# Kernel optimization log

Hardware: AMD Instinct MI355X
Metric: run time of the kernel (lower is better)

Reference implementation:

```python
import jax, jax.numpy as jnp
import numpy as np

IGNORE_LABEL_ID = -100
GRID = 40                 # grid_width
PATH = 6                  # path_token_id
SP_W = 10.0               # spatial_penalty_weight
CONN_W = 5.0              # connectivity_weight
SEQ = GRID * GRID         # 1600
BIG = SEQ                 # sentinel larger than any flat index


def _spatial_penalty(pred):
    """Vectorized version of spatial_connectivity_loss's per-batch python loop.
    For each predicted path token, find the NEXT path token in flat order and
    penalize Manhattan jumps > 1. pred: [B, SEQ] int."""
    B = pred.shape[0]
    mask = pred == PATH                                   # [B,S]
    idx = jnp.arange(SEQ, dtype=jnp.int32)
    cand = jnp.where(mask, idx[None, :], BIG)
    # nxt[b,i] = smallest path index >= i (reverse cumulative min)
    nxt = jax.lax.cummin(cand, axis=1, reverse=True)
    # next path index strictly after i
    nxt_after = jnp.concatenate([nxt[:, 1:], jnp.full((B, 1), BIG, nxt.dtype)], axis=1)
    valid = mask & (nxt_after < BIG)                      # pairs (i, next)
    p2 = jnp.minimum(nxt_after, SEQ - 1)                  # keep indices in-range
    r1, c1 = idx // GRID, idx % GRID
    r2, c2 = p2 // GRID, p2 % GRID
    dist = jnp.abs(r1[None, :] - r2) + jnp.abs(c1[None, :] - c2)
    pen = jnp.where(valid & (dist > 1), (dist - 1).astype(jnp.float32) * SP_W, 0.0)
    return pen.sum() / B


def _connectivity_penalty(pred):
    """Parallel connected-component labeling (min-label propagation) replacing
    the CPU flood fill. pred: [B, SEQ] int."""
    B = pred.shape[0]
    mask = pred.reshape(B, GRID, GRID) == PATH
    idx = jnp.arange(SEQ, dtype=jnp.int32).reshape(GRID, GRID)
    lab0 = jnp.where(mask, idx[None], BIG)

    def prop(lab):
        p = jnp.pad(lab, ((0, 0), (1, 1), (1, 1)), constant_values=BIG)
        nmin = jnp.minimum(jnp.minimum(p[:, :-2, 1:-1], p[:, 2:, 1:-1]),
                           jnp.minimum(p[:, 1:-1, :-2], p[:, 1:-1, 2:]))
        return jnp.where(mask, jnp.minimum(lab, nmin), BIG)

    def cond(st):
        return st[1]

    def body(st):
        lab, _ = st
        new = prop(lab)
        return (new, jnp.any(new != lab))

    lab, _ = jax.lax.while_loop(cond, body, (lab0, jnp.array(True)))
    # a component is counted once at its minimal (root) cell
    comp = (mask & (lab == idx[None])).sum(axis=(1, 2))
    pen = jnp.where(comp > 1, (comp - 1).astype(jnp.float32) * CONN_W, 0.0)
    return pen.sum() / B


def setup_inputs() -> dict:
    key = jax.random.key(0)
    k1, k2, k3, k4, k5 = jax.random.split(key, 5)
    B, S, V = 1024, SEQ, 32
    return {
        "logits": jax.random.normal(k1, (B, S, V), dtype=jnp.float32),
        "labels": jax.random.randint(k2, (B, S), 0, V).astype(jnp.int64),
        "q_halt_logits": jax.random.normal(k3, (B,), dtype=jnp.float32),
        "halted": jax.random.randint(k4, (B,), 0, 2).astype(bool),
        "steps": jax.random.randint(k5, (B,), 0, 16).astype(jnp.int32),
    }


def reference(logits, labels, q_halt_logits, halted, steps):
    # halted/steps feed no-grad metrics only; loss math below matches ACTLossHead.
    mask = labels != IGNORE_LABEL_ID                       # [B,S]
    loss_counts = mask.sum(-1)
    loss_divisor = jnp.maximum(loss_counts, 1)[:, None].astype(logits.dtype)

    pred = jnp.argmax(logits, axis=-1)                     # [B,S]
    is_correct = mask & (pred == labels)
    seq_is_correct = is_correct.sum(-1) == loss_counts     # [B] bool

    # softmax cross entropy with ignore_index, per token
    logp = jax.nn.log_softmax(logits, axis=-1)
    safe_labels = jnp.maximum(labels, 0)
    ce = -jnp.take_along_axis(logp, safe_labels[..., None], axis=-1)[..., 0]
    ce = jnp.where(mask, ce, 0.0)
    lm_loss = (ce / loss_divisor).sum()

    # BCE-with-logits, reduction='sum'
    t = seq_is_correct.astype(logits.dtype)
    x = q_halt_logits
    q_halt_loss = (jnp.maximum(x, 0) - x * t + jnp.log1p(jnp.exp(-jnp.abs(x)))).sum()

    spatial_loss = _spatial_penalty(pred)
    connectivity_loss = _connectivity_penalty(pred)

    total_loss = lm_loss + 0.5 * q_halt_loss + spatial_loss + connectivity_loss
    return total_loss
```

## Files before the change

### kernel.cpp

```cpp
#include <hip/hip_runtime.h>
#include <cstdint>

#define GRIDW   40
#define SEQ     1600
#define NVOCAB  32
#define PATH_ID 6
#define IGNORE_ID (-100)
#define NWORDS  25
#define BLK     256
#define NWAVES  (BLK / 64)
#define TILE_F4 576

__global__ __launch_bounds__(BLK) void act_loss_kernel(
    const float* __restrict__ logits,
    const int*   __restrict__ labels,
    const float* __restrict__ qhalt,
    float*       __restrict__ out,
    int B)
{
    const int b    = blockIdx.x;
    const int tid  = threadIdx.x;
    const int lane = tid & 63;
    const int wid  = tid >> 6;

    __shared__ __align__(16) float4 stage4[NWAVES * TILE_F4];
    __shared__ uint8_t  path[SEQ];
    __shared__ uint64_t words[NWORDS];
    __shared__ int      offs[NWORDS + 1];
    __shared__ int      npath_s;
    __shared__ float    wr_f[NWAVES];
    __shared__ int      wr_i[NWAVES];
    __shared__ int      wr_j[NWAVES];
    __shared__ float    part_a;

    uint16_t* lab = (uint16_t*)stage4;
    uint16_t* pos = (uint16_t*)stage4 + SEQ;

    float ce_sum = 0.0f;
    int   cnt = 0, cor = 0;

    const float4* gbase = (const float4*)(logits + (size_t)b * SEQ * NVOCAB);
    const int*    lbase = labels + (size_t)b * SEQ;

    float4* stg  = stage4 + wid * TILE_F4;
    const float* frow_base = (const float*)stg;

    for (int t = wid; t < SEQ / 64; t += NWAVES) {
        const float4* gp = gbase + (size_t)t * 512;

        float4 g[8];
#pragma unroll
        for (int k = 0; k < 8; ++k)
            g[k] = gp[k * 64 + lane];

        int tok = t * 64 + lane;
        int lbl = lbase[tok];

#pragma unroll
        for (int k = 0; k < 8; ++k)
            stg[(k * 8 + (lane >> 3)) * 9 + (lane & 7)] = g[k];

        float4 x[8];
#pragma unroll
        for (int j = 0; j < 8; ++j)
            x[j] = stg[lane * 9 + j];

        float m = x[0].x; int arg = 0;
#pragma unroll
        for (int j = 0; j < 8; ++j) {
            int i4 = 4 * j;
            if (j > 0 && x[j].x > m) { m = x[j].x; arg = i4; }
            if (x[j].y > m) { m = x[j].y; arg = i4 + 1; }
            if (x[j].z > m) { m = x[j].z; arg = i4 + 2; }
            if (x[j].w > m) { m = x[j].w; arg = i4 + 3; }
        }
        float s0 = 0.f, s1 = 0.f, s2 = 0.f, s3 = 0.f;
#pragma unroll
        for (int j = 0; j < 8; ++j) {
            s0 += __expf(x[j].x - m);
            s1 += __expf(x[j].y - m);
            s2 += __expf(x[j].z - m);
            s3 += __expf(x[j].w - m);
        }
        float s = (s0 + s1) + (s2 + s3);

        bool msk  = (lbl != IGNORE_ID);
        int  slbl = (lbl < 0) ? 0 : lbl;
        float xl = frow_base[lane * 36 + slbl];

        float lse = m + __logf(s);
        ce_sum += msk ? (lse - xl) : 0.0f;
        cnt    += msk ? 1 : 0;
        cor    += (msk && arg == lbl) ? 1 : 0;
        path[tok] = (arg == PATH_ID) ? 1 : 0;
    }
    __syncthreads();

    for (int basei = 0; basei < SEQ; basei += BLK) {
        int idx = basei + tid;
        bool p = (idx < SEQ) ? (path[idx] != 0) : false;
        uint64_t w = __ballot(p);
        int widx = (basei >> 6) + wid;
        if (lane == 0 && widx < NWORDS) words[widx] = w;
    }

    for (int d = 1; d < 64; d <<= 1) {
        ce_sum += __shfl_xor(ce_sum, d);
        cnt    += __shfl_xor(cnt, d);
        cor    += __shfl_xor(cor, d);
    }
    if (lane == 0) { wr_f[wid] = ce_sum; wr_i[wid] = cnt; wr_j[wid] = cor; }
    __syncthreads();

    if (tid == 0) {
        float ce_tot = wr_f[0] + wr_f[1] + wr_f[2] + wr_f[3];
        int   c_tot  = wr_i[0] + wr_i[1] + wr_i[2] + wr_i[3];
        int   k_tot  = wr_j[0] + wr_j[1] + wr_j[2] + wr_j[3];
        float lm = ce_tot / (float)max(c_tot, 1);
        float t  = (k_tot == c_tot) ? 1.0f : 0.0f;
        float xq = qhalt[b];
        float bce = fmaxf(xq, 0.0f) - xq * t + log1pf(expf(-fabsf(xq)));
        part_a = lm + 0.5f * bce;
    }

    if (wid == 0) {
        uint64_t w = (lane < NWORDS) ? words[lane] : 0ull;
        int pc = __popcll(w);
        int c = pc;
        for (int d = 1; d < 32; d <<= 1) {
            int t = __shfl_up(c, d);
            if (lane >= d) c += t;
        }
        if (lane < NWORDS) offs[lane] = c - pc;
        if (lane == NWORDS - 1) { offs[NWORDS] = c; npath_s = c; }
    }
    __syncthreads();

    if (tid < NWORDS) {
        int o = offs[tid];
        uint64_t w = words[tid];
        int basei = tid * 64;
        while (w) {
            int k = __ffsll((unsigned long long)w) - 1;
            pos[o++] = (uint16_t)(basei + k);
            w &= (w - 1);
        }
    }
    __syncthreads();

    const int np = npath_s;
    int sp_units = 0;
    for (int q = tid; q + 1 < np; q += BLK) {
        int i = pos[q], j = pos[q + 1];
        int dist = abs(i / GRIDW - j / GRIDW) + abs(i % GRIDW - j % GRIDW);
        if (dist > 1) sp_units += dist - 1;
    }

    for (int i = tid; i < SEQ; i += BLK)
        lab[i] = path[i] ? (uint16_t)i : (uint16_t)0xFFFF;
    __syncthreads();

    for (;;) {
        int local = 0;
        for (int i = tid; i < SEQ; i += BLK) {
            if (!path[i]) continue;
            int r = i / GRIDW, c = i % GRIDW;
            uint16_t v = lab[i];
            uint16_t nm = v;
            if (r > 0)         { uint16_t u = lab[i - GRIDW]; nm = (u < nm) ? u : nm; }
            if (r < GRIDW - 1) { uint16_t u = lab[i + GRIDW]; nm = (u < nm) ? u : nm; }
            if (c > 0)         { uint16_t u = lab[i - 1];     nm = (u < nm) ? u : nm; }
            if (c < GRIDW - 1) { uint16_t u = lab[i + 1];     nm = (u < nm) ? u : nm; }
            if (nm < v) { lab[i] = nm; local = 1; }
        }
        if (__syncthreads_count(local) == 0) break;
    }

    int comp = 0;
    for (int i = tid; i < SEQ; i += BLK)
        comp += (path[i] && lab[i] == (uint16_t)i) ? 1 : 0;

    for (int d = 1; d < 64; d <<= 1) {
        sp_units += __shfl_xor(sp_units, d);
        comp     += __shfl_xor(comp, d);
    }
    if (lane == 0) { wr_i[wid] = sp_units; wr_j[wid] = comp; }
    __syncthreads();

    if (tid == 0) {
        int sp_tot   = wr_i[0] + wr_i[1] + wr_i[2] + wr_i[3];
        int comp_tot = wr_j[0] + wr_j[1] + wr_j[2] + wr_j[3];
        int conn_units = (comp_tot > 1) ? (comp_tot - 1) : 0;
        float total = part_a +
                      ((float)sp_tot * 10.0f + (float)conn_units * 5.0f) / (float)B;
        atomicAdd(out, total);
    }
}

extern "C" void kernel_launch(void* const* d_in, const int* in_sizes, int n_in,
                              void* d_out, int out_size, void* d_ws, size_t ws_size,
                              hipStream_t stream) {
    const float* logits = (const float*)d_in[0];
    const int*   labels = (const int*)d_in[1];
    const float* qhalt  = (const float*)d_in[2];
    float* out = (float*)d_out;
    const int B = in_sizes[2];

    hipMemsetAsync(out, 0, (size_t)out_size * sizeof(float), stream);
    act_loss_kernel<<<dim3(B), dim3(BLK), 0, stream>>>(logits, labels, qhalt, out, B);
}
```

Baseline: 307.7 us.

## Process two batch rows per 512-thread block with swizzled LDS staging

Doubles the block size to 512 threads and has each block handle two batch rows in sequence. It also replaces the padded LDS transpose with an XOR-swizzled layout, uses nontemporal loads for logits and labels, and builds the path bitmask words with a ballot inside the main loop. The label and position arrays get their own shared buffers instead of aliasing the staging area. Halving the grid may reduce parallelism when the batch is small, and the larger shared footprint may limit occupancy.

```diff
diff --git a/kernel.cpp b/kernel.cpp
--- a/kernel.cpp
+++ b/kernel.cpp
@@ -7,24 +7,27 @@
 #define PATH_ID 6
 #define IGNORE_ID (-100)
 #define NWORDS  25
-#define BLK     256
+#define BLK     512
 #define NWAVES  (BLK / 64)
-#define TILE_F4 576
-
-__global__ __launch_bounds__(BLK) void act_loss_kernel(
+#define ROWS_PER_BLK 2
+
+typedef float f32x4 __attribute__((ext_vector_type(4)));
+
+__global__ __launch_bounds__(BLK, 4) void act_loss_kernel(
     const float* __restrict__ logits,
     const int*   __restrict__ labels,
     const float* __restrict__ qhalt,
     float*       __restrict__ out,
     int B)
 {
-    const int b    = blockIdx.x;
     const int tid  = threadIdx.x;
     const int lane = tid & 63;
     const int wid  = tid >> 6;
 
-    __shared__ __align__(16) float4 stage4[NWAVES * TILE_F4];
+    __shared__ __align__(16) f32x4 stage[NWAVES * 512];
     __shared__ uint8_t  path[SEQ];
+    __shared__ uint16_t lab[SEQ];
+    __shared__ uint16_t pos[SEQ];
     __shared__ uint64_t words[NWORDS];
     __shared__ int      offs[NWORDS + 1];
     __shared__ int      npath_s;
@@ -33,167 +36,170 @@
     __shared__ int      wr_j[NWAVES];
     __shared__ float    part_a;
 
-    uint16_t* lab = (uint16_t*)stage4;
-    uint16_t* pos = (uint16_t*)stage4 + SEQ;
-
-    float ce_sum = 0.0f;
-    int   cnt = 0, cor = 0;
-
-    const float4* gbase = (const float4*)(logits + (size_t)b * SEQ * NVOCAB);
-    const int*    lbase = labels + (size_t)b * SEQ;
-
-    float4* stg  = stage4 + wid * TILE_F4;
-    const float* frow_base = (const float*)stg;
-
-    for (int t = wid; t < SEQ / 64; t += NWAVES) {
-        const float4* gp = gbase + (size_t)t * 512;
-
-        float4 g[8];
-#pragma unroll
-        for (int k = 0; k < 8; ++k)
-            g[k] = gp[k * 64 + lane];
-
-        int tok = t * 64 + lane;
-        int lbl = lbase[tok];
-
-#pragma unroll
-        for (int k = 0; k < 8; ++k)
-            stg[(k * 8 + (lane >> 3)) * 9 + (lane & 7)] = g[k];
-
-        float4 x[8];
-#pragma unroll
-        for (int j = 0; j < 8; ++j)
-            x[j] = stg[lane * 9 + j];
-
-        float m = x[0].x; int arg = 0;
-#pragma unroll
-        for (int j = 0; j < 8; ++j) {
-            int i4 = 4 * j;
-            if (j > 0 && x[j].x > m) { m = x[j].x; arg = i4; }
-            if (x[j].y > m) { m = x[j].y; arg = i4 + 1; }
-            if (x[j].z > m) { m = x[j].z; arg = i4 + 2; }
-            if (x[j].w > m) { m = x[j].w; arg = i4 + 3; }
-        }
-        float s0 = 0.f, s1 = 0.f, s2 = 0.f, s3 = 0.f;
-#pragma unroll
-        for (int j = 0; j < 8; ++j) {
-            s0 += __expf(x[j].x - m);
-            s1 += __expf(x[j].y - m);
-            s2 += __expf(x[j].z - m);
-            s3 += __expf(x[j].w - m);
-        }
-        float s = (s0 + s1) + (s2 + s3);
-
-        bool msk  = (lbl != IGNORE_ID);
-        int  slbl = (lbl < 0) ? 0 : lbl;
-        float xl = frow_base[lane * 36 + slbl];
-
-        float lse = m + __logf(s);
-        ce_sum += msk ? (lse - xl) : 0.0f;
-        cnt    += msk ? 1 : 0;
-        cor    += (msk && arg == lbl) ? 1 : 0;
-        path[tok] = (arg == PATH_ID) ? 1 : 0;
-    }
-    __syncthreads();
-
-    for (int basei = 0; basei < SEQ; basei += BLK) {
-        int idx = basei + tid;
-        bool p = (idx < SEQ) ? (path[idx] != 0) : false;
-        uint64_t w = __ballot(p);
-        int widx = (basei >> 6) + wid;
-        if (lane == 0 && widx < NWORDS) words[widx] = w;
-    }
-
-    for (int d = 1; d < 64; d <<= 1) {
-        ce_sum += __shfl_xor(ce_sum, d);
-        cnt    += __shfl_xor(cnt, d);
-        cor    += __shfl_xor(cor, d);
-    }
-    if (lane == 0) { wr_f[wid] = ce_sum; wr_i[wid] = cnt; wr_j[wid] = cor; }
-    __syncthreads();
-
-    if (tid == 0) {
-        float ce_tot = wr_f[0] + wr_f[1] + wr_f[2] + wr_f[3];
-        int   c_tot  = wr_i[0] + wr_i[1] + wr_i[2] + wr_i[3];
-        int   k_tot  = wr_j[0] + wr_j[1] + wr_j[2] + wr_j[3];
-        float lm = ce_tot / (float)max(c_tot, 1);
-        float t  = (k_tot == c_tot) ? 1.0f : 0.0f;
-        float xq = qhalt[b];
-        float bce = fmaxf(xq, 0.0f) - xq * t + log1pf(expf(-fabsf(xq)));
-        part_a = lm + 0.5f * bce;
-    }
-
-    if (wid == 0) {
-        uint64_t w = (lane < NWORDS) ? words[lane] : 0ull;
-        int pc = __popcll(w);
-        int c = pc;
-        for (int d = 1; d < 32; d <<= 1) {
-            int t = __shfl_up(c, d);
-            if (lane >= d) c += t;
-        }
-        if (lane < NWORDS) offs[lane] = c - pc;
-        if (lane == NWORDS - 1) { offs[NWORDS] = c; npath_s = c; }
-    }
-    __syncthreads();
-
-    if (tid < NWORDS) {
-        int o = offs[tid];
-        uint64_t w = words[tid];
-        int basei = tid * 64;
-        while (w) {
-            int k = __ffsll((unsigned long long)w) - 1;
-            pos[o++] = (uint16_t)(basei + k);
-            w &= (w - 1);
-        }
-    }
-    __syncthreads();
-
-    const int np = npath_s;
-    int sp_units = 0;
-    for (int q = tid; q + 1 < np; q += BLK) {
-        int i = pos[q], j = pos[q + 1];
-        int dist = abs(i / GRIDW - j / GRIDW) + abs(i % GRIDW - j % GRIDW);
-        if (dist > 1) sp_units += dist - 1;
-    }
-
-    for (int i = tid; i < SEQ; i += BLK)
-        lab[i] = path[i] ? (uint16_t)i : (uint16_t)0xFFFF;
-    __syncthreads();
-
-    for (;;) {
-        int local = 0;
-        for (int i = tid; i < SEQ; i += BLK) {
-            if (!path[i]) continue;
-            int r = i / GRIDW, c = i % GRIDW;
-            uint16_t v = lab[i];
-            uint16_t nm = v;
-            if (r > 0)         { uint16_t u = lab[i - GRIDW]; nm = (u < nm) ? u : nm; }
-            if (r < GRIDW - 1) { uint16_t u = lab[i + GRIDW]; nm = (u < nm) ? u : nm; }
-            if (c > 0)         { uint16_t u = lab[i - 1];     nm = (u < nm) ? u : nm; }
-            if (c < GRIDW - 1) { uint16_t u = lab[i + 1];     nm = (u < nm) ? u : nm; }
-            if (nm < v) { lab[i] = nm; local = 1; }
-        }
-        if (__syncthreads_count(local) == 0) break;
-    }
-
-    int comp = 0;
-    for (int i = tid; i < SEQ; i += BLK)
-        comp += (path[i] && lab[i] == (uint16_t)i) ? 1 : 0;
-
-    for (int d = 1; d < 64; d <<= 1) {
-        sp_units += __shfl_xor(sp_units, d);
-        comp     += __shfl_xor(comp, d);
-    }
-    if (lane == 0) { wr_i[wid] = sp_units; wr_j[wid] = comp; }
-    __syncthreads();
-
-    if (tid == 0) {
-        int sp_tot   = wr_i[0] + wr_i[1] + wr_i[2] + wr_i[3];
-        int comp_tot = wr_j[0] + wr_j[1] + wr_j[2] + wr_j[3];
-        int conn_units = (comp_tot > 1) ? (comp_tot - 1) : 0;
-        float total = part_a +
-                      ((float)sp_tot * 10.0f + (float)conn_units * 5.0f) / (float)B;
-        atomicAdd(out, total);
+    f32x4* stg = stage + wid * 512;
+    const float* stf = (const float*)stg;
+
+    for (int r = 0; r < ROWS_PER_BLK; ++r) {
+        const int b = blockIdx.x * ROWS_PER_BLK + r;
+        if (b >= B) break;
+
+        const f32x4* gbase = (const f32x4*)(logits + (size_t)b * SEQ * NVOCAB);
+        const int*   lbase = labels + (size_t)b * SEQ;
+
+        float ce_sum = 0.0f;
+        int   cnt = 0, cor = 0;
+
+#pragma unroll 1
+        for (int tile = wid; tile < SEQ / 64; tile += NWAVES) {
+            const f32x4* gp = gbase + (size_t)tile * 512;
+
+            f32x4 g[8];
+#pragma unroll
+            for (int k = 0; k < 8; ++k)
+                g[k] = __builtin_nontemporal_load(gp + k * 64 + lane);
+
+            int tok = tile * 64 + lane;
+            int lbl = __builtin_nontemporal_load(lbase + tok);
+
+#pragma unroll
+            for (int k = 0; k < 8; ++k) {
+                int t8  = k * 8 + (lane >> 3);
+                int cmp = lane & 7;
+                stg[t8 * 8 + (cmp ^ (t8 & 7))] = g[k];
+            }
+            f32x4 x[8];
+#pragma unroll
+            for (int j = 0; j < 8; ++j)
+                x[j] = stg[lane * 8 + (j ^ (lane & 7))];
+
+            float m = x[0].x; int arg = 0;
+#pragma unroll
+            for (int j = 0; j < 8; ++j) {
+                int i4 = 4 * j;
+                if (j > 0 && x[j].x > m) { m = x[j].x; arg = i4; }
+                if (x[j].y > m) { m = x[j].y; arg = i4 + 1; }
+                if (x[j].z > m) { m = x[j].z; arg = i4 + 2; }
+                if (x[j].w > m) { m = x[j].w; arg = i4 + 3; }
+            }
+            float s0 = 0.f, s1 = 0.f, s2 = 0.f, s3 = 0.f;
+#pragma unroll
+            for (int j = 0; j < 8; ++j) {
+                s0 += __expf(x[j].x - m);
+                s1 += __expf(x[j].y - m);
+                s2 += __expf(x[j].z - m);
+                s3 += __expf(x[j].w - m);
+            }
+            float s = (s0 + s1) + (s2 + s3);
+
+            bool msk  = (lbl != IGNORE_ID);
+            int  slbl = (lbl < 0) ? 0 : lbl;
+            float xl = stf[(lane * 8 + (((slbl >> 2) & 7) ^ (lane & 7))) * 4 + (slbl & 3)];
+
+            float lse = m + __logf(s);
+            ce_sum += msk ? (lse - xl) : 0.0f;
+            cnt    += msk ? 1 : 0;
+            cor    += (msk && arg == lbl) ? 1 : 0;
+
+            bool pf = (arg == PATH_ID);
+            path[tok] = pf ? 1 : 0;
+            uint64_t w = __ballot(pf);
+            if (lane == 0) words[tile] = w;
+        }
+        __syncthreads();
+
+        for (int d = 1; d < 64; d <<= 1) {
+            ce_sum += __shfl_xor(ce_sum, d);
+            cnt    += __shfl_xor(cnt, d);
+            cor    += __shfl_xor(cor, d);
+        }
+        if (lane == 0) { wr_f[wid] = ce_sum; wr_i[wid] = cnt; wr_j[wid] = cor; }
+        __syncthreads();
+
+        if (tid == 0) {
+            float ce_tot = 0.0f; int c_tot = 0, k_tot = 0;
+#pragma unroll
+            for (int v = 0; v < NWAVES; ++v) {
+                ce_tot += wr_f[v]; c_tot += wr_i[v]; k_tot += wr_j[v];
+            }
+            float lm = ce_tot / (float)max(c_tot, 1);
+            float t  = (k_tot == c_tot) ? 1.0f : 0.0f;
+            float xq = qhalt[b];
+            float bce = fmaxf(xq, 0.0f) - xq * t + log1pf(expf(-fabsf(xq)));
+            part_a = lm + 0.5f * bce;
+        }
+
+        if (wid == 0) {
+            uint64_t w = (lane < NWORDS) ? words[lane] : 0ull;
+            int pc = __popcll(w);
+            int c = pc;
+            for (int d = 1; d < 32; d <<= 1) {
+                int t = __shfl_up(c, d);
+                if (lane >= d) c += t;
+            }
+            if (lane < NWORDS) offs[lane] = c - pc;
+            if (lane == NWORDS - 1) { offs[NWORDS] = c; npath_s = c; }
+        }
+        __syncthreads();
+
+        for (int i = tid; i < SEQ; i += BLK)
+            lab[i] = path[i] ? (uint16_t)i : (uint16_t)0xFFFF;
+        if (tid < NWORDS) {
+            int o = offs[tid];
+            uint64_t w = words[tid];
+            int basei = tid * 64;
+            while (w) {
+                int k = __ffsll((unsigned long long)w) - 1;
+                pos[o++] = (uint16_t)(basei + k);
+                w &= (w - 1);
+            }
+        }
+        __syncthreads();
+
+        const int np = npath_s;
+        int sp_units = 0;
+        for (int q = tid; q + 1 < np; q += BLK) {
+            int i = pos[q], j = pos[q + 1];
+            int dist = abs(i / GRIDW - j / GRIDW) + abs(i % GRIDW - j % GRIDW);
+            if (dist > 1) sp_units += dist - 1;
+        }
+
+        for (;;) {
+            int local = 0;
+            for (int i = tid; i < SEQ; i += BLK) {
+                if (!path[i]) continue;
+                int rr = i / GRIDW, cc = i % GRIDW;
+                uint16_t v = lab[i];
+                uint16_t nm = v;
+                if (rr > 0)         { uint16_t u = lab[i - GRIDW]; nm = (u < nm) ? u : nm; }
+                if (rr < GRIDW - 1) { uint16_t u = lab[i + GRIDW]; nm = (u < nm) ? u : nm; }
+                if (cc > 0)         { uint16_t u = lab[i - 1];     nm = (u < nm) ? u : nm; }
+                if (cc < GRIDW - 1) { uint16_t u = lab[i + 1];     nm = (u < nm) ? u : nm; }
+                if (nm < v) { lab[i] = nm; local = 1; }
+            }
+            if (__syncthreads_count(local) == 0) break;
+        }
+
+        int comp = 0;
+        for (int i = tid; i < SEQ; i += BLK)
+            comp += (path[i] && lab[i] == (uint16_t)i) ? 1 : 0;
+
+        for (int d = 1; d < 64; d <<= 1) {
+            sp_units += __shfl_xor(sp_units, d);
+            comp     += __shfl_xor(comp, d);
+        }
+        if (lane == 0) { wr_i[wid] = sp_units; wr_j[wid] = comp; }
+        __syncthreads();
+
+        if (tid == 0) {
+            int sp_tot = 0, comp_tot = 0;
+#pragma unroll
+            for (int v = 0; v < NWAVES; ++v) { sp_tot += wr_i[v]; comp_tot += wr_j[v]; }
+            int conn_units = (comp_tot > 1) ? (comp_tot - 1) : 0;
+            float total = part_a +
+                          ((float)sp_tot * 10.0f + (float)conn_units * 5.0f) / (float)B;
+            atomicAdd(out, total);
+        }
+        __syncthreads();
     }
 }
 
@@ -207,5 +213,6 @@
     const int B = in_sizes[2];
 
     hipMemsetAsync(out, 0, (size_t)out_size * sizeof(float), stream);
-    act_loss_kernel<<<dim3(B), dim3(BLK), 0, stream>>>(logits, labels, qhalt, out, B);
+    const int nblk = (B + ROWS_PER_BLK - 1) / ROWS_PER_BLK;
+    act_loss_kernel<<<dim3(nblk), dim3(BLK), 0, stream>>>(logits, labels, qhalt, out, B);
 }
```

Measured after the change: 284.8 us. 1.08x faster.
